# Optimization experiments

Hardware: AMD Instinct MI355X
Metric: run time of the kernel (lower is better)

Reference implementation:

```python
import jax, jax.numpy as jnp
import numpy as np

EPS = 1e-12  # matches torch F.normalize default eps in spectral_norm


def _l2norm(v):
    return v / jnp.maximum(jnp.linalg.norm(v), EPS)


def _spectral_norm(W, u):
    # One power-iteration step (torch spectral_norm training behavior).
    # u, v are treated as constants w.r.t. gradients.
    v = jax.lax.stop_gradient(_l2norm(W.T @ u))
    u2 = jax.lax.stop_gradient(_l2norm(W @ v))
    sigma = jnp.einsum('o,oi,i->', u2, W, v)
    return W / sigma


def setup_inputs() -> dict:
    key = jax.random.key(0)
    ks = jax.random.split(key, 8)
    B, C, N = 8, 512, 2048
    d = C // 8
    return {
        'x':  jax.random.normal(ks[0], (B, C, N), dtype=jnp.float32),
        'Wq': jax.random.normal(ks[1], (d, C), dtype=jnp.float32) * (1.0 / np.sqrt(C)),
        'Wk': jax.random.normal(ks[2], (d, C), dtype=jnp.float32) * (1.0 / np.sqrt(C)),
        'Wv': jax.random.normal(ks[3], (C, C), dtype=jnp.float32) * (1.0 / np.sqrt(C)),
        'uq': jax.random.normal(ks[4], (d,), dtype=jnp.float32),
        'uk': jax.random.normal(ks[5], (d,), dtype=jnp.float32),
        'uv': jax.random.normal(ks[6], (C,), dtype=jnp.float32),
        'gamma': jax.random.normal(ks[7], (1,), dtype=jnp.float32) * 0.1,
    }


def reference(x, Wq, Wk, Wv, uq, uk, uv, gamma):
    # x: [B, C, N]
    f = jnp.einsum('oi,bin->bon', _spectral_norm(Wq, uq), x)  # [B, C/8, N]
    g = jnp.einsum('oi,bin->bon', _spectral_norm(Wk, uk), x)  # [B, C/8, N]
    h = jnp.einsum('oi,bin->bon', _spectral_norm(Wv, uv), x)  # [B, C, N]
    scores = jnp.einsum('bdn,bdm->bnm', f, g)                 # f^T g: [B, N, N]
    beta = jax.nn.softmax(scores, axis=1)                      # softmax over dim=1
    o = gamma[0] * jnp.einsum('bcn,bnm->bcm', h, beta) + x    # [B, C, N]
    return o
```

## Files before the change

### kernel.cpp

```cpp
#include <hip/hip_runtime.h>
#include <hip/hip_bf16.h>
#include <math.h>

#define B_ 8
#define C_ 512
#define N_ 2048
#define D_ 64
#define O_ 640

typedef __bf16 bf16x8 __attribute__((ext_vector_type(8)));
typedef float f32x4 __attribute__((ext_vector_type(4)));
typedef unsigned short ushort8_t __attribute__((ext_vector_type(8)));
typedef unsigned short ushort4_t __attribute__((ext_vector_type(4)));

__device__ __forceinline__ unsigned short f2bf(float f) {
    unsigned int u = __builtin_bit_cast(unsigned int, f);
    u += 0x7fffu + ((u >> 16) & 1u);
    return (unsigned short)(u >> 16);
}

__device__ __forceinline__ unsigned short f2bf_hw(float f) {
    __bf16 h = (__bf16)f;
    return __builtin_bit_cast(unsigned short, h);
}

__device__ __forceinline__ float fastexp(float x) {
    return exp2f(x * 1.44269504088896340736f);
}

union FragU { ushort8_t u; bf16x8 b; };

__device__ __forceinline__ bf16x8 ldfrag(const unsigned short* p) {
    FragU t; t.u = *(const ushort8_t*)p; return t.b;
}

__device__ __forceinline__ bf16x8 asfrag(ushort8_t u) {
    FragU t; t.u = u; return t.b;
}

__device__ __forceinline__ void gload_lds16(const unsigned short* g, unsigned short* l) {
    __builtin_amdgcn_global_load_lds((const __attribute__((address_space(1))) void*)g,
                                     (__attribute__((address_space(3))) void*)l,
                                     16, 0, 0);
}

__global__ __launch_bounds__(512) void k_colvec(const float* __restrict__ Wq,
                                                const float* __restrict__ Wk,
                                                const float* __restrict__ Wv,
                                                const float* __restrict__ uq,
                                                const float* __restrict__ uk,
                                                const float* __restrict__ uv,
                                                float* __restrict__ tpart) {
    int which = blockIdx.y, oq = blockIdx.x;
    const float* W; const float* u; int R;
    if (which == 0)      { W = Wq; u = uq; R = 64;  }
    else if (which == 1) { W = Wk; u = uk; R = 64;  }
    else                 { W = Wv; u = uv; R = 512; }
    int chunk = R >> 2;
    int i = threadIdx.x;
    float s = 0.f;
    int o0 = oq * chunk, o1 = o0 + chunk;
    for (int o = o0; o < o1; ++o) s += W[(size_t)o * 512 + i] * u[o];
    tpart[((which << 2) + oq) * 512 + i] = s;
}

__global__ __launch_bounds__(512) void k_trow(const float* __restrict__ tpart,
                                              float* __restrict__ tvec,
                                              float* __restrict__ t2) {
    int which = blockIdx.x, i = threadIdx.x;
    const float* tp = tpart + (which << 2) * 512;
    float s = tp[i] + tp[512 + i] + tp[1024 + i] + tp[1536 + i];
    tvec[which * 512 + i] = s;
    __shared__ float red[512];
    red[i] = s * s; __syncthreads();
    for (int st = 256; st > 0; st >>= 1) { if (i < st) red[i] += red[i + st]; __syncthreads(); }
    if (i == 0) t2[which] = red[0];
}

__global__ __launch_bounds__(256) void k_rowvec(const float* __restrict__ Wq,
                                                const float* __restrict__ Wk,
                                                const float* __restrict__ Wv,
                                                const float* __restrict__ tvec,
                                                float* __restrict__ wpart) {
    int which = blockIdx.y;
    const float* W; int R;
    if (which == 0)      { W = Wq; R = 64;  }
    else if (which == 1) { W = Wk; R = 64;  }
    else                 { W = Wv; R = 512; }
    int tid = threadIdx.x, lane = tid & 63, wv = tid >> 6;
    int row = blockIdx.x * 4 + wv;
    float ps = 0.f;
    if (row < R) {
        const float4* wr_ = (const float4*)(W + (size_t)row * 512);
        const float4* tv = (const float4*)(tvec + which * 512);
        float4 a0 = wr_[lane * 2], a1 = wr_[lane * 2 + 1];
        float4 b0 = tv[lane * 2], b1 = tv[lane * 2 + 1];
        float s = a0.x * b0.x + a0.y * b0.y + a0.z * b0.z + a0.w * b0.w
                + a1.x * b1.x + a1.y * b1.y + a1.z * b1.z + a1.w * b1.w;
        #pragma unroll
        for (int off = 1; off < 64; off <<= 1) s += __shfl_xor(s, off, 64);
        ps = s * s;
    }
    __shared__ float red[4];
    if (lane == 0) red[wv] = ps;
    __syncthreads();
    if (tid == 0) wpart[which * 128 + blockIdx.x] = red[0] + red[1] + red[2] + red[3];
}

__global__ __launch_bounds__(128) void k_scale(const float* __restrict__ wpart,
                                               const float* __restrict__ t2,
                                               float* __restrict__ scales) {
    int which = blockIdx.x, tid = threadIdx.x;
    float s = wpart[which * 128 + tid];
    #pragma unroll
    for (int off = 1; off < 64; off <<= 1) s += __shfl_xor(s, off, 64);
    __shared__ float r2[2];
    if ((tid & 63) == 0) r2[tid >> 6] = s;
    __syncthreads();
    if (tid == 0) scales[which] = sqrtf(t2[which] / fmaxf(r2[0] + r2[1], 1e-24f));
}

__global__ __launch_bounds__(256) void k_wconv(const float* __restrict__ Wq,
                                               const float* __restrict__ Wk,
                                               const float* __restrict__ Wv,
                                               const float* __restrict__ scales,
                                               unsigned short* __restrict__ Wb) {
    int gid = blockIdx.x * 256 + threadIdx.x;
    int e0 = gid * 8;
    int o = e0 >> 9, i = e0 & 511;
    const float* src; float sc;
    if (o < 64)       { src = Wq + (size_t)o * 512;         sc = scales[0]; }
    else if (o < 128) { src = Wk + (size_t)(o - 64) * 512;  sc = scales[1]; }
    else              { src = Wv + (size_t)(o - 128) * 512; sc = scales[2]; }
    float4 v0 = *(const float4*)(src + i), v1 = *(const float4*)(src + i + 4);
    ushort8_t u;
    u[0] = f2bf(v0.x * sc); u[1] = f2bf(v0.y * sc); u[2] = f2bf(v0.z * sc); u[3] = f2bf(v0.w * sc);
    u[4] = f2bf(v1.x * sc); u[5] = f2bf(v1.y * sc); u[6] = f2bf(v1.z * sc); u[7] = f2bf(v1.w * sc);
    *(ushort8_t*)&Wb[(size_t)o * 512 + i] = u;
}

__global__ __launch_bounds__(256) void k_transpose(const float* __restrict__ x,
                                                   unsigned short* __restrict__ xT) {
    __shared__ float tile[64][33];
    int b = blockIdx.z;
    int n0 = blockIdx.x * 32, c0 = blockIdx.y * 64;
    int tx = threadIdx.x, ty = threadIdx.y;
    #pragma unroll
    for (int k = 0; k < 8; ++k) {
        int c = ty + k * 8;
        tile[c][tx] = x[((size_t)b * C_ + c0 + c) * N_ + n0 + tx];
    }
    __syncthreads();
    #pragma unroll
    for (int k = 0; k < 4; ++k) {
        int n = ty + k * 8;
        unsigned int p = (unsigned int)f2bf(tile[tx * 2][n]) |
                         ((unsigned int)f2bf(tile[tx * 2 + 1][n]) << 16);
        *(unsigned int*)&xT[((size_t)b * N_ + n0 + n) * C_ + c0 + tx * 2] = p;
    }
}

__global__ __launch_bounds__(256) void k_proj(const unsigned short* __restrict__ xT,
                                              const unsigned short* __restrict__ Wb,
                                              unsigned short* __restrict__ fT,
                                              unsigned short* __restrict__ gT,
                                              unsigned short* __restrict__ hb) {
    int bid = blockIdx.x;
    int xcd = bid & 7, r = bid >> 3;
    int o_t = r % 5;
    int sub = (r / 5) & 1;
    int b = r / 10;
    int n0 = (xcd * 2 + sub) * 128, o0 = o_t * 128;

    int tid = threadIdx.x, lane = tid & 63, w = tid >> 6;
    int wr = w >> 1, wc = w & 1;
    __shared__ __align__(16) unsigned short Sh[16384];
    unsigned short* As = Sh;
    unsigned short* Bs = Sh + 8192;
    f32x4 zero = {0.f, 0.f, 0.f, 0.f};
    f32x4 acc[4][4];
    #pragma unroll
    for (int i = 0; i < 4; ++i)
        #pragma unroll
        for (int j = 0; j < 4; ++j) acc[i][j] = zero;
    int r8 = lane >> 3, sl = lane & 7;
    int scol = (sl ^ r8) * 8;

    for (int kt = 0; kt < 8; ++kt) {
        #pragma unroll
        for (int q = 0; q < 4; ++q) {
            int chunk = w * 4 + q;
            int row = chunk * 8 + r8;
            gload_lds16(xT + ((size_t)b * N_ + n0 + row) * C_ + kt * 64 + scol, &As[chunk * 512]);
            gload_lds16(Wb + (size_t)(o0 + row) * C_ + kt * 64 + scol, &Bs[chunk * 512]);
        }
        __syncthreads();
        int kg = lane >> 4, r16 = lane & 15;
        #pragma unroll
        for (int kk = 0; kk < 2; ++kk) {
            int sw = kk * 4 + kg;
            bf16x8 af[4];
            #pragma unroll
            for (int i = 0; i < 4; ++i) {
                int row = wr * 64 + i * 16 + r16;
                af[i] = ldfrag(&As[row * 64 + (sw ^ (row & 7)) * 8]);
            }
            #pragma unroll
            for (int j = 0; j < 4; ++j) {
                int row = wc * 64 + j * 16 + r16;
                bf16x8 bv = ldfrag(&Bs[row * 64 + (sw ^ (row & 7)) * 8]);
                #pragma unroll
                for (int i = 0; i < 4; ++i)
                    acc[i][j] = __builtin_amdgcn_mfma_f32_16x16x32_bf16(af[i], bv, acc[i][j], 0, 0, 0);
            }
        }
        __syncthreads();
    }

    unsigned short* St = Sh;
    if (o0 == 0) {
        #pragma unroll
        for (int p = 0; p < 2; ++p) {
            if (wc == p) {
                #pragma unroll
                for (int i = 0; i < 4; ++i)
                    #pragma unroll
                    for (int j = 0; j < 4; ++j)
                        #pragma unroll
                        for (int r2_ = 0; r2_ < 4; ++r2_)
                            St[(wr * 64 + i * 16 + (lane >> 4) * 4 + r2_) * 72 + j * 16 + (lane & 15)] = f2bf(acc[i][j][r2_]);
            }
            __syncthreads();
            unsigned short* dst = p == 0 ? fT : gT;
            #pragma unroll
            for (int it = 0; it < 4; ++it) {
                int row = it * 32 + (tid >> 3);
                *(ushort8_t*)&dst[((size_t)b * N_ + n0 + row) * D_ + (tid & 7) * 8] =
                    *(ushort8_t*)&St[row * 72 + (tid & 7) * 8];
            }
            __syncthreads();
        }
    } else {
        int ho0 = o0 - 128;
        #pragma unroll
        for (int p = 0; p < 2; ++p) {
            if (wc == p) {
                #pragma unroll
                for (int i = 0; i < 4; ++i)
                    #pragma unroll
                    for (int j = 0; j < 4; ++j)
                        #pragma unroll
                        for (int r2_ = 0; r2_ < 4; ++r2_)
                            St[(j * 16 + (lane & 15)) * 136 + wr * 64 + i * 16 + (lane >> 4) * 4 + r2_] = f2bf(acc[i][j][r2_]);
            }
            __syncthreads();
            #pragma unroll
            for (int it = 0; it < 4; ++it) {
                int row = it * 16 + (tid >> 4);
                *(ushort8_t*)&hb[((size_t)b * C_ + ho0 + p * 64 + row) * N_ + n0 + (tid & 15) * 8] =
                    *(ushort8_t*)&St[row * 136 + (tid & 15) * 8];
            }
            __syncthreads();
        }
    }
}

__global__ __launch_bounds__(256) void k_stats(const unsigned short* __restrict__ fT,
                                               const unsigned short* __restrict__ gT,
                                               float* __restrict__ colmax,
                                               float* __restrict__ colsinv) {
    int bid = blockIdx.x;
    int b = bid & 7, m0 = (bid >> 3) * 16;
    int tid = threadIdx.x, lane = tid & 63, w = tid >> 6;
    int mcol = m0 + (lane & 15);
    const unsigned short* gbase = gT + ((size_t)b * N_ + mcol) * D_ + (lane >> 4) * 8;
    bf16x8 g0 = ldfrag(gbase);
    bf16x8 g1 = ldfrag(gbase + 32);

    float mx = -1e30f, sm = 0.f;
    for (int nt = w * 32; nt < w * 32 + 32; ++nt) {
        const unsigned short* abase = fT + ((size_t)b * N_ + nt * 16 + (lane & 15)) * D_ + (lane >> 4) * 8;
        f32x4 s = {0.f, 0.f, 0.f, 0.f};
        s = __builtin_amdgcn_mfma_f32_16x16x32_bf16(ldfrag(abase), g0, s, 0, 0, 0);
        s = __builtin_amdgcn_mfma_f32_16x16x32_bf16(ldfrag(abase + 32), g1, s, 0, 0, 0);
        float tm = fmaxf(fmaxf(s[0], s[1]), fmaxf(s[2], s[3]));
        float nm = fmaxf(mx, tm);
        float c = fastexp(mx - nm);
        sm = sm * c + fastexp(s[0] - nm) + fastexp(s[1] - nm) + fastexp(s[2] - nm) + fastexp(s[3] - nm);
        mx = nm;
    }
    #pragma unroll
    for (int off = 16; off < 64; off <<= 1) {
        float omx = __shfl_xor(mx, off, 64);
        float osm = __shfl_xor(sm, off, 64);
        float nm = fmaxf(mx, omx);
        sm = sm * fastexp(mx - nm) + osm * fastexp(omx - nm);
        mx = nm;
    }
    __shared__ float lmx[4][16], lsm[4][16];
    if ((lane >> 4) == 0) { lmx[w][lane & 15] = mx; lsm[w][lane & 15] = sm; }
    __syncthreads();
    if (tid < 16) {
        float M = lmx[0][tid], S = lsm[0][tid];
        #pragma unroll
        for (int q = 1; q < 4; ++q) {
            float om = lmx[q][tid], os = lsm[q][tid];
            float nm = fmaxf(M, om);
            S = S * fastexp(M - nm) + os * fastexp(om - nm);
            M = nm;
        }
        colmax[(size_t)b * N_ + m0 + tid] = M;
        colsinv[(size_t)b * N_ + m0 + tid] = 1.0f / S;
    }
}

__global__ __launch_bounds__(512, 4) void k_av(const unsigned short* __restrict__ fT,
                                               const unsigned short* __restrict__ gT,
                                               const unsigned short* __restrict__ hb,
                                               const float* __restrict__ colmax,
                                               const float* __restrict__ colsinv,
                                               const float* __restrict__ x,
                                               const float* __restrict__ gamma,
                                               float* __restrict__ out) {
    __shared__ __align__(16) unsigned short HB[16384];
    __shared__ __align__(16) unsigned short BS[2][4096];

    const int NT = N_ / 64;
    int bid = blockIdx.x;
    int xg = bid & 7, sidx = bid >> 3;
    int mi = sidx & 31, gh = sidx >> 5;
    int g = xg + 8 * gh;
    int b = g >> 1, ch = g & 1;
    int m0 = mi * 64, c0 = ch * 256;

    int tid = threadIdx.x, lane = tid & 63, w = tid >> 6;
    int nw = w & 3, mh = w >> 2;
    int l15 = lane & 15, lq = lane >> 4;
    int r8 = lane >> 3, sl = lane & 7;
    int scol = (sl ^ r8) * 8;

    const float LOG2E = 1.44269504088896340736f;
    bf16x8 gf[2][2];
    float off_[2];
    #pragma unroll
    for (int j = 0; j < 2; ++j) {
        int m = m0 + mh * 32 + j * 16 + l15;
        #pragma unroll
        for (int kd = 0; kd < 2; ++kd)
            gf[j][kd] = ldfrag(gT + ((size_t)b * N_ + m) * D_ + kd * 32 + lq * 8);
        off_[j] = log2f(colsinv[(size_t)b * N_ + m]) - colmax[(size_t)b * N_ + m] * LOG2E;
    }

    f32x4 zero = {0.f, 0.f, 0.f, 0.f};
    f32x4 acc[2][4];
    #pragma unroll
    for (int i = 0; i < 2; ++i)
        #pragma unroll
        for (int j = 0; j < 4; ++j) acc[i][j] = zero;

    const unsigned short* fbase = fT + ((size_t)b * N_) * D_;
    const unsigned short* hbase = hb + ((size_t)b * C_ + c0) * N_;

    ushort8_t hreg0, hreg1, hreg2, hreg3;
    ushort8_t freg0, freg1;

    auto HLOAD = [&](int kt) {
        hreg0 = *(const ushort8_t*)(hbase + (size_t)((w * 4 + 0) * 8 + r8) * N_ + kt * 64 + scol);
        hreg1 = *(const ushort8_t*)(hbase + (size_t)((w * 4 + 1) * 8 + r8) * N_ + kt * 64 + scol);
        hreg2 = *(const ushort8_t*)(hbase + (size_t)((w * 4 + 2) * 8 + r8) * N_ + kt * 64 + scol);
        hreg3 = *(const ushort8_t*)(hbase + (size_t)((w * 4 + 3) * 8 + r8) * N_ + kt * 64 + scol);
    };
    auto HWRITE = [&]() {
        *(ushort8_t*)&HB[(w * 4 + 0) * 512 + lane * 8] = hreg0;
        *(ushort8_t*)&HB[(w * 4 + 1) * 512 + lane * 8] = hreg1;
        *(ushort8_t*)&HB[(w * 4 + 2) * 512 + lane * 8] = hreg2;
        *(ushort8_t*)&HB[(w * 4 + 3) * 512 + lane * 8] = hreg3;
    };
    auto FLOAD = [&](int kt) {
        const unsigned short* fp = fbase + ((size_t)kt * 64 + nw * 16 + l15) * D_ + lq * 8;
        freg0 = *(const ushort8_t*)fp;
        freg1 = *(const ushort8_t*)(fp + 32);
    };
    auto SPHASE = [&](int p) {
        bf16x8 af0 = asfrag(freg0);
        bf16x8 af1 = asfrag(freg1);
        #pragma unroll
        for (int j = 0; j < 2; ++j) {
            f32x4 sv = zero;
            sv = __builtin_amdgcn_mfma_f32_16x16x32_bf16(af0, gf[j][0], sv, 0, 0, 0);
            sv = __builtin_amdgcn_mfma_f32_16x16x32_bf16(af1, gf[j][1], sv, 0, 0, 0);
            int mrel = mh * 32 + j * 16 + l15;
            ushort4_t pk;
            #pragma unroll
            for (int r = 0; r < 4; ++r)
                pk[r] = f2bf_hw(exp2f(fmaf(sv[r], LOG2E, off_[j])));
            int nt = nw * 16 + lq * 4;
            *(ushort4_t*)&BS[p][mrel * 64 + (((nt >> 3) ^ (mrel & 7)) * 8) + (nt & 7)] = pk;
        }
    };
    auto PVPHASE = [&](int p) {
        __builtin_amdgcn_s_setprio(1);
        #pragma unroll
        for (int kk = 0; kk < 2; ++kk) {
            int ng = kk * 4 + lq;
            bf16x8 pa[2];
            #pragma unroll
            for (int i = 0; i < 2; ++i) {
                int mr = mh * 32 + i * 16 + l15;
                pa[i] = ldfrag(&BS[p][mr * 64 + ((ng ^ (mr & 7)) * 8)]);
            }
            #pragma unroll
            for (int j = 0; j < 4; ++j) {
                int cr = nw * 64 + j * 16 + l15;
                bf16x8 hv = ldfrag(&HB[cr * 64 + ((ng ^ (cr & 7)) * 8)]);
                #pragma unroll
                for (int i = 0; i < 2; ++i)
                    acc[i][j] = __builtin_amdgcn_mfma_f32_16x16x32_bf16(pa[i], hv, acc[i][j], 0, 0, 0);
            }
        }
        __builtin_amdgcn_s_setprio(0);
    };

    HLOAD(0);
    FLOAD(0);
    asm volatile("s_waitcnt vmcnt(0)" ::: "memory");
    __builtin_amdgcn_sched_barrier(0);
    HWRITE();
    SPHASE(0);
    asm volatile("s_waitcnt lgkmcnt(0)" ::: "memory");
    __builtin_amdgcn_sched_barrier(0);
    __builtin_amdgcn_s_barrier();
    __builtin_amdgcn_sched_barrier(0);

    #pragma unroll 1
    for (int kt = 0; kt < NT; ++kt) {
        int p = kt & 1;
        if (kt + 1 < NT) {
            HLOAD(kt + 1);
            FLOAD(kt + 1);
            __builtin_amdgcn_sched_barrier(0);
        }
        PVPHASE(p);
        if (kt + 1 < NT) {
            asm volatile("s_waitcnt vmcnt(0)" ::: "memory");
            __builtin_amdgcn_sched_barrier(0);
            __builtin_amdgcn_s_barrier();
            __builtin_amdgcn_sched_barrier(0);
            HWRITE();
            SPHASE(p ^ 1);
            asm volatile("s_waitcnt lgkmcnt(0)" ::: "memory");
            __builtin_amdgcn_sched_barrier(0);
            __builtin_amdgcn_s_barrier();
            __builtin_amdgcn_sched_barrier(0);
        }
    }

    float gv = gamma[0];
    #pragma unroll
    for (int i = 0; i < 2; ++i) {
        int mabs = m0 + mh * 32 + i * 16 + lq * 4;
        #pragma unroll
        for (int j = 0; j < 4; ++j) {
            int cabs = c0 + nw * 64 + j * 16 + l15;
            size_t base = ((size_t)b * C_ + cabs) * N_ + mabs;
            float4 xv = *(const float4*)(x + base);
            float4 ov;
            ov.x = gv * acc[i][j][0] + xv.x;
            ov.y = gv * acc[i][j][1] + xv.y;
            ov.z = gv * acc[i][j][2] + xv.z;
            ov.w = gv * acc[i][j][3] + xv.w;
            *(float4*)(out + base) = ov;
        }
    }
}

extern "C" void kernel_launch(void* const* d_in, const int* in_sizes, int n_in,
                              void* d_out, int out_size, void* d_ws, size_t ws_size,
                              hipStream_t stream) {
    const float* x     = (const float*)d_in[0];
    const float* Wq    = (const float*)d_in[1];
    const float* Wk    = (const float*)d_in[2];
    const float* Wv    = (const float*)d_in[3];
    const float* uq    = (const float*)d_in[4];
    const float* uk    = (const float*)d_in[5];
    const float* uv    = (const float*)d_in[6];
    const float* gamma = (const float*)d_in[7];
    float* out = (float*)d_out;

    char* wsb = (char*)d_ws;
    float* scales         = (float*)wsb;
    unsigned short* xT    = (unsigned short*)(wsb + 256);
    unsigned short* fT    = xT + (size_t)B_ * N_ * C_;
    unsigned short* gT    = fT + (size_t)B_ * N_ * D_;
    unsigned short* hb    = gT + (size_t)B_ * N_ * D_;
    float* colmax         = (float*)(hb + (size_t)B_ * C_ * N_);
    float* colsinv        = colmax + (size_t)B_ * N_;
    float* tpart          = colsinv + (size_t)B_ * N_;
    float* tvec           = tpart + 3 * 4 * 512;
    float* t2             = tvec + 3 * 512;
    float* wpart          = t2 + 16;
    unsigned short* Wb    = (unsigned short*)(wpart + 3 * 128);

    k_colvec<<<dim3(4, 3), 512, 0, stream>>>(Wq, Wk, Wv, uq, uk, uv, tpart);
    k_trow<<<3, 512, 0, stream>>>(tpart, tvec, t2);
    k_rowvec<<<dim3(128, 3), 256, 0, stream>>>(Wq, Wk, Wv, tvec, wpart);
    k_scale<<<3, 128, 0, stream>>>(wpart, t2, scales);
    k_wconv<<<O_ * C_ / (256 * 8), 256, 0, stream>>>(Wq, Wk, Wv, scales, Wb);
    k_transpose<<<dim3(N_ / 32, C_ / 64, B_), dim3(32, 8), 0, stream>>>(x, xT);
    k_proj<<<640, 256, 0, stream>>>(xT, Wb, fT, gT, hb);
    k_stats<<<1024, 256, 0, stream>>>(fT, gT, colmax, colsinv);
    k_av<<<512, 512, 0, stream>>>(fT, gT, hb, colmax, colsinv, x, gamma, out);
}
```

Measured before the change: 174.9 us.

## Halve k_av output tile and load H fragments directly from global

The attention-times-value kernel now uses a 32-column output tile instead of 64, doubling the grid to 1024 blocks. H fragments are read straight from global memory into registers instead of being staged through a swizzled LDS buffer, and the P buffer is single-buffered. Launch bounds are raised to target more waves per SIMD. This shrinks LDS use and register pressure to raise occupancy, but each H tile is now reused across only 32 columns, so H global traffic doubles and the exp/S computation is spread thinner.

```diff
diff --git a/kernel.cpp b/kernel.cpp
--- a/kernel.cpp
+++ b/kernel.cpp
@@ -314,7 +314,7 @@
     }
 }
 
-__global__ __launch_bounds__(512, 4) void k_av(const unsigned short* __restrict__ fT,
+__global__ __launch_bounds__(512, 6) void k_av(const unsigned short* __restrict__ fT,
                                                const unsigned short* __restrict__ gT,
                                                const unsigned short* __restrict__ hb,
                                                const float* __restrict__ colmax,
@@ -322,111 +322,84 @@
                                                const float* __restrict__ x,
                                                const float* __restrict__ gamma,
                                                float* __restrict__ out) {
-    __shared__ __align__(16) unsigned short HB[16384];
-    __shared__ __align__(16) unsigned short BS[2][4096];
+    __shared__ __align__(16) unsigned short BS[2048];
 
     const int NT = N_ / 64;
     int bid = blockIdx.x;
     int xg = bid & 7, sidx = bid >> 3;
-    int mi = sidx & 31, gh = sidx >> 5;
+    int mi = sidx & 63, gh = sidx >> 6;
     int g = xg + 8 * gh;
     int b = g >> 1, ch = g & 1;
-    int m0 = mi * 64, c0 = ch * 256;
+    int m0 = mi * 32, c0 = ch * 256;
 
     int tid = threadIdx.x, lane = tid & 63, w = tid >> 6;
     int nw = w & 3, mh = w >> 2;
     int l15 = lane & 15, lq = lane >> 4;
-    int r8 = lane >> 3, sl = lane & 7;
-    int scol = (sl ^ r8) * 8;
 
     const float LOG2E = 1.44269504088896340736f;
-    bf16x8 gf[2][2];
-    float off_[2];
-    #pragma unroll
-    for (int j = 0; j < 2; ++j) {
-        int m = m0 + mh * 32 + j * 16 + l15;
-        #pragma unroll
-        for (int kd = 0; kd < 2; ++kd)
-            gf[j][kd] = ldfrag(gT + ((size_t)b * N_ + m) * D_ + kd * 32 + lq * 8);
-        off_[j] = log2f(colsinv[(size_t)b * N_ + m]) - colmax[(size_t)b * N_ + m] * LOG2E;
+    bf16x8 gf0, gf1;
+    float off_;
+    {
+        int m = m0 + mh * 16 + l15;
+        gf0 = ldfrag(gT + ((size_t)b * N_ + m) * D_ + lq * 8);
+        gf1 = ldfrag(gT + ((size_t)b * N_ + m) * D_ + 32 + lq * 8);
+        off_ = log2f(colsinv[(size_t)b * N_ + m]) - colmax[(size_t)b * N_ + m] * LOG2E;
     }
 
     f32x4 zero = {0.f, 0.f, 0.f, 0.f};
-    f32x4 acc[2][4];
-    #pragma unroll
-    for (int i = 0; i < 2; ++i)
-        #pragma unroll
-        for (int j = 0; j < 4; ++j) acc[i][j] = zero;
+    f32x4 acc[4];
+    #pragma unroll
+    for (int j = 0; j < 4; ++j) acc[j] = zero;
 
     const unsigned short* fbase = fT + ((size_t)b * N_) * D_;
     const unsigned short* hbase = hb + ((size_t)b * C_ + c0) * N_;
-
-    ushort8_t hreg0, hreg1, hreg2, hreg3;
+    int hoff[4];
+    #pragma unroll
+    for (int j = 0; j < 4; ++j) {
+        int cr = nw * 64 + j * 16 + l15;
+        hoff[j] = cr * N_ + lq * 8;
+    }
+
+    int mr = mh * 16 + l15;
     ushort8_t freg0, freg1;
 
-    auto HLOAD = [&](int kt) {
-        hreg0 = *(const ushort8_t*)(hbase + (size_t)((w * 4 + 0) * 8 + r8) * N_ + kt * 64 + scol);
-        hreg1 = *(const ushort8_t*)(hbase + (size_t)((w * 4 + 1) * 8 + r8) * N_ + kt * 64 + scol);
-        hreg2 = *(const ushort8_t*)(hbase + (size_t)((w * 4 + 2) * 8 + r8) * N_ + kt * 64 + scol);
-        hreg3 = *(const ushort8_t*)(hbase + (size_t)((w * 4 + 3) * 8 + r8) * N_ + kt * 64 + scol);
-    };
-    auto HWRITE = [&]() {
-        *(ushort8_t*)&HB[(w * 4 + 0) * 512 + lane * 8] = hreg0;
-        *(ushort8_t*)&HB[(w * 4 + 1) * 512 + lane * 8] = hreg1;
-        *(ushort8_t*)&HB[(w * 4 + 2) * 512 + lane * 8] = hreg2;
-        *(ushort8_t*)&HB[(w * 4 + 3) * 512 + lane * 8] = hreg3;
-    };
     auto FLOAD = [&](int kt) {
         const unsigned short* fp = fbase + ((size_t)kt * 64 + nw * 16 + l15) * D_ + lq * 8;
         freg0 = *(const ushort8_t*)fp;
         freg1 = *(const ushort8_t*)(fp + 32);
     };
-    auto SPHASE = [&](int p) {
-        bf16x8 af0 = asfrag(freg0);
-        bf16x8 af1 = asfrag(freg1);
-        #pragma unroll
-        for (int j = 0; j < 2; ++j) {
-            f32x4 sv = zero;
-            sv = __builtin_amdgcn_mfma_f32_16x16x32_bf16(af0, gf[j][0], sv, 0, 0, 0);
-            sv = __builtin_amdgcn_mfma_f32_16x16x32_bf16(af1, gf[j][1], sv, 0, 0, 0);
-            int mrel = mh * 32 + j * 16 + l15;
-            ushort4_t pk;
-            #pragma unroll
-            for (int r = 0; r < 4; ++r)
-                pk[r] = f2bf_hw(exp2f(fmaf(sv[r], LOG2E, off_[j])));
-            int nt = nw * 16 + lq * 4;
-            *(ushort4_t*)&BS[p][mrel * 64 + (((nt >> 3) ^ (mrel & 7)) * 8) + (nt & 7)] = pk;
-        }
+    auto SPHASE = [&]() {
+        f32x4 sv = zero;
+        sv = __builtin_amdgcn_mfma_f32_16x16x32_bf16(asfrag(freg0), gf0, sv, 0, 0, 0);
+        sv = __builtin_amdgcn_mfma_f32_16x16x32_bf16(asfrag(freg1), gf1, sv, 0, 0, 0);
+        ushort4_t pk;
+        #pragma unroll
+        for (int r = 0; r < 4; ++r)
+            pk[r] = f2bf_hw(exp2f(fmaf(sv[r], LOG2E, off_)));
+        int nt = nw * 16 + lq * 4;
+        *(ushort4_t*)&BS[mr * 64 + (((nt >> 3) ^ (mr & 7)) * 8) + (nt & 7)] = pk;
     };
-    auto PVPHASE = [&](int p) {
+    auto PVPHASE = [&](int kt) {
+        ushort8_t hv[2][4];
+        #pragma unroll
+        for (int kk = 0; kk < 2; ++kk)
+            #pragma unroll
+            for (int j = 0; j < 4; ++j)
+                hv[kk][j] = *(const ushort8_t*)(hbase + hoff[j] + kt * 64 + kk * 32);
         __builtin_amdgcn_s_setprio(1);
         #pragma unroll
         for (int kk = 0; kk < 2; ++kk) {
             int ng = kk * 4 + lq;
-            bf16x8 pa[2];
-            #pragma unroll
-            for (int i = 0; i < 2; ++i) {
-                int mr = mh * 32 + i * 16 + l15;
-                pa[i] = ldfrag(&BS[p][mr * 64 + ((ng ^ (mr & 7)) * 8)]);
-            }
-            #pragma unroll
-            for (int j = 0; j < 4; ++j) {
-                int cr = nw * 64 + j * 16 + l15;
-                bf16x8 hv = ldfrag(&HB[cr * 64 + ((ng ^ (cr & 7)) * 8)]);
-                #pragma unroll
-                for (int i = 0; i < 2; ++i)
-                    acc[i][j] = __builtin_amdgcn_mfma_f32_16x16x32_bf16(pa[i], hv, acc[i][j], 0, 0, 0);
-            }
+            bf16x8 pa = ldfrag(&BS[mr * 64 + ((ng ^ (mr & 7)) * 8)]);
+            #pragma unroll
+            for (int j = 0; j < 4; ++j)
+                acc[j] = __builtin_amdgcn_mfma_f32_16x16x32_bf16(pa, asfrag(hv[kk][j]), acc[j], 0, 0, 0);
         }
         __builtin_amdgcn_s_setprio(0);
     };
 
-    HLOAD(0);
     FLOAD(0);
-    asm volatile("s_waitcnt vmcnt(0)" ::: "memory");
-    __builtin_amdgcn_sched_barrier(0);
-    HWRITE();
-    SPHASE(0);
+    SPHASE();
     asm volatile("s_waitcnt lgkmcnt(0)" ::: "memory");
     __builtin_amdgcn_sched_barrier(0);
     __builtin_amdgcn_s_barrier();
@@ -434,20 +407,13 @@
 
     #pragma unroll 1
     for (int kt = 0; kt < NT; ++kt) {
-        int p = kt & 1;
+        if (kt + 1 < NT) FLOAD(kt + 1);
+        PVPHASE(kt);
+        __builtin_amdgcn_sched_barrier(0);
+        __builtin_amdgcn_s_barrier();
+        __builtin_amdgcn_sched_barrier(0);
         if (kt + 1 < NT) {
-            HLOAD(kt + 1);
-            FLOAD(kt + 1);
-            __builtin_amdgcn_sched_barrier(0);
-        }
-        PVPHASE(p);
-        if (kt + 1 < NT) {
-            asm volatile("s_waitcnt vmcnt(0)" ::: "memory");
-            __builtin_amdgcn_sched_barrier(0);
-            __builtin_amdgcn_s_barrier();
-            __builtin_amdgcn_sched_barrier(0);
-            HWRITE();
-            SPHASE(p ^ 1);
+            SPHASE();
             asm volatile("s_waitcnt lgkmcnt(0)" ::: "memory");
             __builtin_amdgcn_sched_barrier(0);
             __builtin_amdgcn_s_barrier();
@@ -456,21 +422,18 @@
     }
 
     float gv = gamma[0];
-    #pragma unroll
-    for (int i = 0; i < 2; ++i) {
-        int mabs = m0 + mh * 32 + i * 16 + lq * 4;
-        #pragma unroll
-        for (int j = 0; j < 4; ++j) {
-            int cabs = c0 + nw * 64 + j * 16 + l15;
-            size_t base = ((size_t)b * C_ + cabs) * N_ + mabs;
-            float4 xv = *(const float4*)(x + base);
-            float4 ov;
-            ov.x = gv * acc[i][j][0] + xv.x;
-            ov.y = gv * acc[i][j][1] + xv.y;
-            ov.z = gv * acc[i][j][2] + xv.z;
-            ov.w = gv * acc[i][j][3] + xv.w;
-            *(float4*)(out + base) = ov;
-        }
+    int mabs = m0 + mh * 16 + lq * 4;
+    #pragma unroll
+    for (int j = 0; j < 4; ++j) {
+        int cabs = c0 + nw * 64 + j * 16 + l15;
+        size_t base = ((size_t)b * C_ + cabs) * N_ + mabs;
+        float4 xv = *(const float4*)(x + base);
+        float4 ov;
+        ov.x = gv * acc[j][0] + xv.x;
+        ov.y = gv * acc[j][1] + xv.y;
+        ov.z = gv * acc[j][2] + xv.z;
+        ov.w = gv * acc[j][3] + xv.w;
+        *(float4*)(out + base) = ov;
     }
 }
 
@@ -509,5 +472,5 @@
     k_transpose<<<dim3(N_ / 32, C_ / 64, B_), dim3(32, 8), 0, stream>>>(x, xT);
     k_proj<<<640, 256, 0, stream>>>(xT, Wb, fT, gT, hb);
     k_stats<<<1024, 256, 0, stream>>>(fT, gT, colmax, colsinv);
-    k_av<<<512, 512, 0, stream>>>(fT, gT, hb, colmax, colsinv, x, gamma, out);
-}
+    k_av<<<1024, 512, 0, stream>>>(fT, gT, hb, colmax, colsinv, x, gamma, out);
+}
```

After: 458.4 us. +162.0%, slower.
